# Kernel tuning notes

Hardware: AMD Instinct MI355X
Metric: run time of the kernel (lower is better)

Reference implementation:

```python
import jax, jax.numpy as jnp
import numpy as np

NINPUT = 16
NHIDDEN = 256
NHAGE = 256
NOUT = 8
NSTEP = 501
BATCH = 256
FP_ITERS = 100  # Picard iterations replacing scipy.fsolve equilibrium solve


def setup_inputs() -> dict:
    key = jax.random.key(0)
    ks = jax.random.split(key, 14)
    def rn(k, shape, s):
        return jax.random.normal(k, shape, dtype=jnp.float32) * s
    D = NINPUT * NHIDDEN + NHIDDEN * NHIDDEN + NHIDDEN
    return {
        "u": rn(ks[0], (BATCH, NSTEP, NINPUT + 1), 1.0),
        # aging GRU (PyTorch nn.GRU, 1 layer, batch_first)
        "gru_Wih": rn(ks[1], (3 * NHAGE, NINPUT + 1), 0.05),
        "gru_Whh": rn(ks[2], (3 * NHAGE, NHAGE), 0.05),
        "gru_bih": rn(ks[3], (3 * NHAGE,), 0.05),
        "gru_bhh": rn(ks[4], (3 * NHAGE,), 0.05),
        # linearage: nhidden_age -> D (small scale so dparams are perturbations)
        "Wage": rn(ks[5], (D, NHAGE), 0.01),
        "bage": rn(ks[6], (D,), 0.01),
        # base RNN cell params (tanh cell: tanh(A x + B u + C))
        "Wih": rn(ks[7], (NHIDDEN, NINPUT), 0.05),
        "Whh": rn(ks[8], (NHIDDEN, NHIDDEN), 0.05),
        "bih": rn(ks[9], (NHIDDEN,), 0.05),
        "bhh": rn(ks[10], (NHIDDEN,), 0.05),
        "tau": rn(ks[11], (NHIDDEN,), 0.1),
        # output head
        "Wout": rn(ks[12], (NOUT, NHIDDEN), 0.05),
        "bout": rn(ks[13], (NOUT,), 0.05),
    }


def reference(u, gru_Wih, gru_Whh, gru_bih, gru_bhh, Wage, bage,
              Wih, Whh, bih, bhh, tau, Wout, bout):
    B, T, _ = u.shape
    nI, nH = NINPUT, NHIDDEN

    # ---- aging GRU over full input (feature dim == ninput+1), h0 = 0 ----
    def gru_step(h, xt):
        gi = xt @ gru_Wih.T + gru_bih        # [B, 3*Hage]
        gh = h @ gru_Whh.T + gru_bhh
        ir, iz, inn = jnp.split(gi, 3, axis=-1)
        hr, hz, hn = jnp.split(gh, 3, axis=-1)
        r = jax.nn.sigmoid(ir + hr)
        z = jax.nn.sigmoid(iz + hz)
        n = jnp.tanh(inn + r * hn)
        return (1.0 - z) * n + z * h, None

    h0 = jnp.zeros((B, NHAGE), u.dtype)
    hT, _ = jax.lax.scan(gru_step, h0, jnp.swapaxes(u, 0, 1))
    dparams = hT @ Wage.T + bage             # [B, D]

    # ---- per-sample parameter perturbations (param_update, rnn branch) ----
    Dwu = dparams[:, : nI * nH].reshape(B, nH, nI)
    Dwr = dparams[:, nI * nH : nI * nH + nH * nH].reshape(B, nH, nH)
    Dbu = dparams[:, nI * nH + nH * nH :]
    A = Whh + Dwr                            # [B, H, H]
    Bm = Wih + Dwu                           # [B, H, I]
    C = bih + bhh + Dbu                      # [B, H]

    un = u[:, :, :nI]                        # ODE drive signal
    et = jnp.exp(tau)
    Bu = jnp.einsum('bhi,bti->bth', Bm, un)  # precompute B@u(t): [B, T, H]

    # ---- equilibrium init (rnnzero): x = exp(tau) * tanh(A x + B u0 + C) ----
    def fp(i, x):
        return et * jnp.tanh(jnp.einsum('bhk,bk->bh', A, x) + Bu[:, 0] + C)
    x0 = jax.lax.fori_loop(0, FP_ITERS, fp, jnp.zeros((B, nH), u.dtype))

    # ---- fixed-step Euler on integer grid t=0..T-1 (dt=1); u(t_k)=u[:,k] ----
    def euler(x, bu_k):
        xn = x + jnp.tanh(jnp.einsum('bhk,bk->bh', A, x) + bu_k + C) - x / et
        return xn, xn
    _, xs = jax.lax.scan(euler, x0, jnp.swapaxes(Bu[:, :-1], 0, 1))
    traj = jnp.swapaxes(jnp.concatenate([x0[None], xs], axis=0), 0, 1)  # [B,T,H]

    return traj @ Wout.T + bout              # [B, T, noutput]
```

## Files before the change

### kernel.cpp

```cpp
#include <hip/hip_runtime.h>
#include <hip/hip_bf16.h>

#define BATCH  256
#define TSTEPS 501
#define NIN1   17
#define NH     256
#define DPAR   69888
#define KAUG   288
#define HKAUG  144
#define FPIT   100

typedef _Float16 f16;
typedef f16   f16x2  __attribute__((ext_vector_type(2)));
typedef f16   f16x8  __attribute__((ext_vector_type(8)));
typedef short bf16x8 __attribute__((ext_vector_type(8)));
typedef float f32x4  __attribute__((ext_vector_type(4)));

__device__ __forceinline__ float dot2(unsigned w, unsigned v, float c) {
#if __has_builtin(__builtin_amdgcn_fdot2)
  return __builtin_amdgcn_fdot2(__builtin_bit_cast(f16x2, w), __builtin_bit_cast(f16x2, v), c, false);
#else
  f16x2 a = __builtin_bit_cast(f16x2, w), b = __builtin_bit_cast(f16x2, v);
  return c + (float)a[0] * (float)b[0] + (float)a[1] * (float)b[1];
#endif
}

__device__ __forceinline__ unsigned packh2(float a, float b) {
  f16x2 v; v[0] = (f16)a; v[1] = (f16)b;
  return __builtin_bit_cast(unsigned, v);
}

__device__ __forceinline__ short f2bf(float x) {
  __hip_bfloat16 b = __float2bfloat16(x);
  return __builtin_bit_cast(short, b);
}
__device__ __forceinline__ float bfs2f(short s) {
  return __bfloat162float(__builtin_bit_cast(__hip_bfloat16, s));
}

__device__ __forceinline__ float sigm(float x) { return 1.f / (1.f + __expf(-x)); }
__device__ __forceinline__ float tanh_f(float x) {
  float e = __expf(2.f * x);
  return 1.f - 2.f / (e + 1.f);
}

__global__ __launch_bounds__(512, 1) void gru_kernel(
    const float* __restrict__ u,
    const float* __restrict__ gWih,
    const float* __restrict__ gWhh,
    const float* __restrict__ gbih,
    const float* __restrict__ gbhh,
    short* __restrict__ A2)
{
  const int b   = blockIdx.x;
  const int tid = threadIdx.x;
  const int j   = tid & 255;
  const int hf  = tid >> 8;

  __shared__ __align__(16) unsigned vecu[KAUG / 2];
  __shared__ float part_r[NH], part_z[NH], part_nh[NH], part_ni[NH];
  __shared__ __align__(16) f16 ubuf[TSTEPS * NIN1 + 15];

  {
    const float* ub = u + (size_t)b * TSTEPS * NIN1;
    for (int idx = tid; idx < TSTEPS * NIN1; idx += 512)
      ubuf[idx] = (f16)ub[idx];
  }

  unsigned wr[72], wz[72], wnh[72], wni[9];

  auto augw = [&](int g, int k) -> float {
    if (k < NH) return gWhh[g * NH + k];
    if (k < NH + NIN1) return gWih[g * NIN1 + (k - NH)];
    return 0.f;
  };

#pragma unroll
  for (int p = 0; p < 72; ++p) {
    int k = hf * HKAUG + 2 * p;
    wr[p] = packh2(augw(j, k), augw(j, k + 1));
    wz[p] = packh2(augw(j + 256, k), augw(j + 256, k + 1));
    float n0 = (k     < NH) ? gWhh[(j + 512) * NH + k]     : 0.f;
    float n1 = (k + 1 < NH) ? gWhh[(j + 512) * NH + k + 1] : 0.f;
    wnh[p] = packh2(n0, n1);
  }
#pragma unroll
  for (int p = 0; p < 9; ++p) {
    float a = 0.f, c = 0.f;
    if (hf == 1) {
      a = gWih[(j + 512) * NIN1 + 2 * p];
      if (2 * p + 1 < NIN1) c = gWih[(j + 512) * NIN1 + 2 * p + 1];
    }
    wni[p] = packh2(a, c);
  }
  const float bias_r  = gbih[j]       + gbhh[j];
  const float bias_z  = gbih[j + 256] + gbhh[j + 256];
  const float bias_in = gbih[j + 512];
  const float bias_hn = gbhh[j + 512];

  float h = 0.f;
  {
    f16* vech = (f16*)vecu;
    if (hf == 0) vech[j] = (f16)0.f;
    else if (j < 32) vech[NH + j] = (f16)0.f;
  }
  __syncthreads();
  if (hf == 0 && j < NIN1) ((f16*)vecu)[NH + j] = ubuf[j];
  __syncthreads();

  for (int t = 0; t < TSTEPS; ++t) {
    f16 xnext = (f16)0.f;
    if (hf == 0 && j < NIN1 && t + 1 < TSTEPS)
      xnext = ubuf[(t + 1) * NIN1 + j];

    float accR = 0.f, accZ = 0.f, accNH = 0.f, accNI = 0.f;
    const uint4* v4 = (const uint4*)(vecu + hf * (HKAUG / 2));
#pragma unroll
    for (int c = 0; c < 18; ++c) {
      uint4 v = v4[c];
      accR  = dot2(wr[4 * c + 0], v.x, accR);
      accR  = dot2(wr[4 * c + 1], v.y, accR);
      accR  = dot2(wr[4 * c + 2], v.z, accR);
      accR  = dot2(wr[4 * c + 3], v.w, accR);
      accZ  = dot2(wz[4 * c + 0], v.x, accZ);
      accZ  = dot2(wz[4 * c + 1], v.y, accZ);
      accZ  = dot2(wz[4 * c + 2], v.z, accZ);
      accZ  = dot2(wz[4 * c + 3], v.w, accZ);
      accNH = dot2(wnh[4 * c + 0], v.x, accNH);
      accNH = dot2(wnh[4 * c + 1], v.y, accNH);
      accNH = dot2(wnh[4 * c + 2], v.z, accNH);
      accNH = dot2(wnh[4 * c + 3], v.w, accNH);
    }
    if (hf == 1) {
      const uint4* vi = (const uint4*)(vecu + 128);
      uint4 va = vi[0], vb = vi[1];
      accNI = dot2(wni[0], va.x, accNI);
      accNI = dot2(wni[1], va.y, accNI);
      accNI = dot2(wni[2], va.z, accNI);
      accNI = dot2(wni[3], va.w, accNI);
      accNI = dot2(wni[4], vb.x, accNI);
      accNI = dot2(wni[5], vb.y, accNI);
      accNI = dot2(wni[6], vb.z, accNI);
      accNI = dot2(wni[7], vb.w, accNI);
      accNI = dot2(wni[8], vecu[136], accNI);
      part_r[j] = accR; part_z[j] = accZ; part_nh[j] = accNH; part_ni[j] = accNI;
    }
    __syncthreads();
    if (hf == 0) {
      float rp  = accR  + part_r[j]  + bias_r;
      float zp  = accZ  + part_z[j]  + bias_z;
      float hn  = accNH + part_nh[j] + bias_hn;
      float inn = part_ni[j] + bias_in;
      float r = sigm(rp), z = sigm(zp);
      float n = tanh_f(inn + r * hn);
      h = (1.f - z) * n + z * h;
      f16* vech = (f16*)vecu;
      vech[j] = (f16)h;
      if (j < NIN1) vech[NH + j] = xnext;
    }
    __syncthreads();
  }

  if (hf == 0) {
    short hi = f2bf(h);
    A2[(size_t)b * 512 + j]       = hi;
    A2[(size_t)b * 512 + 256 + j] = f2bf(h - bfs2f(hi));
  }
}

__global__ __launch_bounds__(256, 2) void gemm_kernel(
    const short* __restrict__ A2,
    const float* __restrict__ Wage,
    const float* __restrict__ bage,
    const float* __restrict__ Wih,
    const float* __restrict__ Whh,
    const float* __restrict__ bih,
    const float* __restrict__ bhh,
    f16* __restrict__ dp, int mb, int nb)
{
  __shared__ __align__(16) short As[128 * 40];
  __shared__ __align__(16) short Bs[128 * 40];
  const int tid = threadIdx.x;
  const int n0 = blockIdx.x * 128, m0 = blockIdx.y * 128;
  const int w = tid >> 6, l = tid & 63;
  const int wm = w & 1, wn = w >> 1;
  const int lm = l & 15, lq = l >> 4;

  f32x4 acc[4][4] = {};

  for (int k0 = 0; k0 < 512; k0 += 32) {
    const int ksrc = k0 & 255;
#pragma unroll
    for (int r = 0; r < 2; ++r) {
      int idx = r * 256 + tid;
      int row = idx >> 2, q = idx & 3;
      int rowg = mb + m0 + row; if (rowg > 255) rowg = 255;
      *((uint4*)(As + row * 40 + q * 8)) =
          *((const uint4*)(A2 + (size_t)rowg * 512 + k0 + q * 8));
      const float* wsrc = Wage + (size_t)(n0 + row) * 256 + ksrc + q * 8;
      f32x4 w0 = *((const f32x4*)wsrc);
      f32x4 w1 = *((const f32x4*)(wsrc + 4));
      bf16x8 pk;
      pk[0] = f2bf(w0[0]); pk[1] = f2bf(w0[1]); pk[2] = f2bf(w0[2]); pk[3] = f2bf(w0[3]);
      pk[4] = f2bf(w1[0]); pk[5] = f2bf(w1[1]); pk[6] = f2bf(w1[2]); pk[7] = f2bf(w1[3]);
      *((bf16x8*)(Bs + row * 40 + q * 8)) = pk;
    }
    __syncthreads();
    bf16x8 af[4], bfr[4];
#pragma unroll
    for (int i = 0; i < 4; ++i)
      af[i] = *((const bf16x8*)(As + (wm * 64 + i * 16 + lm) * 40 + lq * 8));
#pragma unroll
    for (int i = 0; i < 4; ++i)
      bfr[i] = *((const bf16x8*)(Bs + (wn * 64 + i * 16 + lm) * 40 + lq * 8));
#pragma unroll
    for (int i = 0; i < 4; ++i)
#pragma unroll
      for (int jn = 0; jn < 4; ++jn)
        acc[i][jn] = __builtin_amdgcn_mfma_f32_16x16x32_bf16(af[i], bfr[jn], acc[i][jn], 0, 0, 0);
    __syncthreads();
  }

  float addv[4];
#pragma unroll
  for (int jn = 0; jn < 4; ++jn) {
    int d = n0 + wn * 64 + jn * 16 + lm;
    float a = bage[d];
    if (d < 4096)       a += Wih[d];
    else if (d < 69632) a += Whh[d - 4096];
    else                a += bih[d - 69632] + bhh[d - 69632];
    addv[jn] = a;
  }

#pragma unroll
  for (int i = 0; i < 4; ++i)
#pragma unroll
    for (int jn = 0; jn < 4; ++jn)
#pragma unroll
      for (int rr = 0; rr < 4; ++rr) {
        int mloc = m0 + wm * 64 + i * 16 + lq * 4 + rr;
        int n = n0 + wn * 64 + jn * 16 + lm;
        if (mloc < nb)
          dp[(size_t)mloc * DPAR + n] = (f16)(acc[i][jn][rr] + addv[jn]);
      }
}

__global__ __launch_bounds__(256, 1) void dyn_kernel(
    const f16* __restrict__ dp, int mb,
    const float* __restrict__ u,
    const float* __restrict__ tau,
    const float* __restrict__ Wout,
    const float* __restrict__ bout,
    float* __restrict__ out)
{
  const int b = mb + blockIdx.x;
  const int j = threadIdx.x;
  const f16* __restrict__ base = dp + (size_t)blockIdx.x * DPAR;

  __shared__ __align__(16) unsigned xbuf[2][128];
  __shared__ __align__(16) unsigned uf[TSTEPS * 8];
  __shared__ __align__(16) float ob[TSTEPS * 8];

  {
    f16* uf16 = (f16*)uf;
    const float* ub = u + (size_t)b * TSTEPS * NIN1;
    for (int idx = j; idx < TSTEPS * 16; idx += 256) {
      int t = idx >> 4, i = idx & 15;
      uf16[idx] = (f16)ub[t * NIN1 + i];
    }
  }

  uint4 Ah[32];
#pragma unroll
  for (int c = 0; c < 32; ++c)
    Ah[c] = *((const uint4*)(base + 4096 + j * 256 + c * 8));
  uint4 Bh0 = *((const uint4*)(base + j * 16));
  uint4 Bh1 = *((const uint4*)(base + j * 16 + 8));
  const float Cc = (float)base[69632 + j];
  const float et = __expf(tau[j]);
  const float inv_et = 1.f / et;

  const int l = j & 63, wv = j >> 6;
  const int po = 2 * wv + (l >> 5), ps = l & 31;
  uint4 wseg;
  {
    const float* wp = Wout + po * 256 + ps * 8;
    wseg.x = packh2(wp[0], wp[1]); wseg.y = packh2(wp[2], wp[3]);
    wseg.z = packh2(wp[4], wp[5]); wseg.w = packh2(wp[6], wp[7]);
  }
  const float bo = bout[po];

  if (j < 128) { xbuf[0][j] = 0u; xbuf[1][j] = 0u; }
  __syncthreads();

  auto bu_at = [&](int t) -> float {
    const uint4* up = (const uint4*)(uf + t * 8);
    uint4 ua = up[0], ub4 = up[1];
    float s0 = dot2(Bh0.x, ua.x, 0.f);  s0 = dot2(Bh0.y, ua.y, s0);
    s0 = dot2(Bh0.z, ua.z, s0);         s0 = dot2(Bh0.w, ua.w, s0);
    float s1 = dot2(Bh1.x, ub4.x, 0.f); s1 = dot2(Bh1.y, ub4.y, s1);
    s1 = dot2(Bh1.z, ub4.z, s1);        s1 = dot2(Bh1.w, ub4.w, s1);
    return s0 + s1;
  };
  const float bu0 = bu_at(0);

  int cur = 0;
  float x = 0.f;
  for (int it = 0; it < FPIT; ++it) {
    float a0 = 0.f, a1 = 0.f, a2 = 0.f, a3 = 0.f;
    const uint4* xp = (const uint4*)xbuf[cur];
#pragma unroll
    for (int c = 0; c < 32; ++c) {
      uint4 v = xp[c];
      a0 = dot2(Ah[c].x, v.x, a0);
      a1 = dot2(Ah[c].y, v.y, a1);
      a2 = dot2(Ah[c].z, v.z, a2);
      a3 = dot2(Ah[c].w, v.w, a3);
    }
    x = et * tanh_f(bu0 + Cc + ((a0 + a1) + (a2 + a3)));
    ((f16*)xbuf[cur ^ 1])[j] = (f16)x;
    __syncthreads();
    cur ^= 1;
  }

  auto project = [&](int t) {
    const uint4* xp = (const uint4*)xbuf[cur];
    uint4 v = xp[ps];
    float p = dot2(wseg.x, v.x, 0.f);
    p = dot2(wseg.y, v.y, p);
    p = dot2(wseg.z, v.z, p);
    p = dot2(wseg.w, v.w, p);
    p += __shfl_down(p, 16, 32);
    p += __shfl_down(p, 8, 32);
    p += __shfl_down(p, 4, 32);
    p += __shfl_down(p, 2, 32);
    p += __shfl_down(p, 1, 32);
    if (ps == 0) ob[t * 8 + po] = p + bo;
  };

  for (int k = 0; k < TSTEPS - 1; ++k) {
    float bu = bu_at(k);
    float a0 = 0.f, a1 = 0.f, a2 = 0.f, a3 = 0.f;
    const uint4* xp = (const uint4*)xbuf[cur];
#pragma unroll
    for (int c = 0; c < 32; ++c) {
      uint4 v = xp[c];
      a0 = dot2(Ah[c].x, v.x, a0);
      a1 = dot2(Ah[c].y, v.y, a1);
      a2 = dot2(Ah[c].z, v.z, a2);
      a3 = dot2(Ah[c].w, v.w, a3);
    }
    float xn = x + tanh_f(bu + Cc + ((a0 + a1) + (a2 + a3))) - x * inv_et;
    ((f16*)xbuf[cur ^ 1])[j] = (f16)xn;
    project(k);
    x = xn;
    __syncthreads();
    cur ^= 1;
  }
  project(TSTEPS - 1);
  __syncthreads();

  {
    float* og = out + (size_t)b * TSTEPS * 8;
    for (int idx = j; idx < TSTEPS * 8; idx += 256) og[idx] = ob[idx];
  }
}

extern "C" void kernel_launch(void* const* d_in, const int* in_sizes, int n_in,
                              void* d_out, int out_size, void* d_ws, size_t ws_size,
                              hipStream_t stream)
{
  const float* u    = (const float*)d_in[0];
  const float* gWih = (const float*)d_in[1];
  const float* gWhh = (const float*)d_in[2];
  const float* gbih = (const float*)d_in[3];
  const float* gbhh = (const float*)d_in[4];
  const float* Wage = (const float*)d_in[5];
  const float* bage = (const float*)d_in[6];
  const float* Wih  = (const float*)d_in[7];
  const float* Whh  = (const float*)d_in[8];
  const float* bih  = (const float*)d_in[9];
  const float* bhh  = (const float*)d_in[10];
  const float* tau  = (const float*)d_in[11];
  const float* Wout = (const float*)d_in[12];
  const float* bout = (const float*)d_in[13];
  float* out = (float*)d_out;

  const size_t A2_BYTES = (size_t)BATCH * 512 * 2;
  size_t a2_off = (ws_size > A2_BYTES + 4096)
                    ? ((ws_size - A2_BYTES) & ~(size_t)255) : 0;
  short* A2 = (short*)((char*)d_ws + a2_off);
  f16* dp = (f16*)d_ws;

  int bpc = (int)(a2_off / ((size_t)DPAR * sizeof(f16)));
  if (bpc < 1)     bpc = 1;
  if (bpc > BATCH) bpc = BATCH;

  gru_kernel<<<BATCH, 512, 0, stream>>>(u, gWih, gWhh, gbih, gbhh, A2);

  for (int mb = 0; mb < BATCH; mb += bpc) {
    int nb = BATCH - mb; if (nb > bpc) nb = bpc;
    dim3 gg(DPAR / 128, (nb + 127) / 128);
    gemm_kernel<<<gg, 256, 0, stream>>>(A2, Wage, bage, Wih, Whh, bih, bhh, dp, mb, nb);
    dyn_kernel<<<nb, 256, 0, stream>>>(dp, mb, u, tau, Wout, bout, out);
  }
}
```

Baseline: 1.551 ms.

## Split GRU recurrence K dimension across four thread groups per block

The GRU kernel now runs 1024 threads per block instead of 512. Each of four 256-thread groups handles a quarter of the augmented K range and writes partial sums to shared memory, where they are reduced. This halves per-thread register weights and the serial dot-product chain per timestep, aiming to cut per-step latency in the sequential recurrence. The cost is more LDS traffic, a larger reduction, and the input-gate weights moved to LDS; a 1024-thread block with many registers may pressure occupancy.

Measured after the change: 1.877 ms. 1.21x slower.

```diff
diff --git a/kernel.cpp b/kernel.cpp
--- a/kernel.cpp
+++ b/kernel.cpp
@@ -7,7 +7,6 @@
 #define NH     256
 #define DPAR   69888
 #define KAUG   288
-#define HKAUG  144
 #define FPIT   100
 
 typedef _Float16 f16;
@@ -44,7 +43,7 @@
   return 1.f - 2.f / (e + 1.f);
 }
 
-__global__ __launch_bounds__(512, 1) void gru_kernel(
+__global__ __launch_bounds__(1024, 1) void gru_kernel(
     const float* __restrict__ u,
     const float* __restrict__ gWih,
     const float* __restrict__ gWhh,
@@ -55,19 +54,18 @@
   const int b   = blockIdx.x;
   const int tid = threadIdx.x;
   const int j   = tid & 255;
-  const int hf  = tid >> 8;
+  const int q   = tid >> 8;
 
   __shared__ __align__(16) unsigned vecu[KAUG / 2];
-  __shared__ float part_r[NH], part_z[NH], part_nh[NH], part_ni[NH];
+  __shared__ float part_r[4][NH], part_z[4][NH], part_nh[4][NH], part_ni[NH];
   __shared__ __align__(16) f16 ubuf[TSTEPS * NIN1 + 15];
+  __shared__ unsigned wniLDS[NH * 9];
 
   {
     const float* ub = u + (size_t)b * TSTEPS * NIN1;
-    for (int idx = tid; idx < TSTEPS * NIN1; idx += 512)
+    for (int idx = tid; idx < TSTEPS * NIN1; idx += 1024)
       ubuf[idx] = (f16)ub[idx];
   }
-
-  unsigned wr[72], wz[72], wnh[72], wni[9];
 
   auto augw = [&](int g, int k) -> float {
     if (k < NH) return gWhh[g * NH + k];
@@ -75,48 +73,49 @@
     return 0.f;
   };
 
-#pragma unroll
-  for (int p = 0; p < 72; ++p) {
-    int k = hf * HKAUG + 2 * p;
+  unsigned wr[36], wz[36], wnh[36];
+  const int k0q = 72 * q;
+#pragma unroll
+  for (int p = 0; p < 36; ++p) {
+    int k = k0q + 2 * p;
     wr[p] = packh2(augw(j, k), augw(j, k + 1));
     wz[p] = packh2(augw(j + 256, k), augw(j + 256, k + 1));
     float n0 = (k     < NH) ? gWhh[(j + 512) * NH + k]     : 0.f;
     float n1 = (k + 1 < NH) ? gWhh[(j + 512) * NH + k + 1] : 0.f;
     wnh[p] = packh2(n0, n1);
   }
-#pragma unroll
-  for (int p = 0; p < 9; ++p) {
-    float a = 0.f, c = 0.f;
-    if (hf == 1) {
-      a = gWih[(j + 512) * NIN1 + 2 * p];
-      if (2 * p + 1 < NIN1) c = gWih[(j + 512) * NIN1 + 2 * p + 1];
-    }
-    wni[p] = packh2(a, c);
-  }
-  const float bias_r  = gbih[j]       + gbhh[j];
-  const float bias_z  = gbih[j + 256] + gbhh[j + 256];
-  const float bias_in = gbih[j + 512];
-  const float bias_hn = gbhh[j + 512];
+
+  float bias_own;
+  if      (q == 0) bias_own = gbih[j]       + gbhh[j];
+  else if (q == 1) bias_own = gbih[j + 256] + gbhh[j + 256];
+  else if (q == 2) bias_own = gbhh[j + 512];
+  else             bias_own = gbih[j + 512];
+
+  if (q == 3) {
+#pragma unroll
+    for (int p = 0; p < 9; ++p) {
+      float a = gWih[(j + 512) * NIN1 + 2 * p];
+      float c = (2 * p + 1 < NIN1) ? gWih[(j + 512) * NIN1 + 2 * p + 1] : 0.f;
+      wniLDS[j * 9 + p] = packh2(a, c);
+    }
+  }
+
+  if (q == 0) ((f16*)vecu)[j] = (f16)0.f;
+  if (q == 1 && j < 32) ((f16*)vecu)[NH + j] = (f16)0.f;
+  __syncthreads();
+  if (q == 0 && j < NIN1) ((f16*)vecu)[NH + j] = ubuf[j];
+  __syncthreads();
 
   float h = 0.f;
-  {
-    f16* vech = (f16*)vecu;
-    if (hf == 0) vech[j] = (f16)0.f;
-    else if (j < 32) vech[NH + j] = (f16)0.f;
-  }
-  __syncthreads();
-  if (hf == 0 && j < NIN1) ((f16*)vecu)[NH + j] = ubuf[j];
-  __syncthreads();
-
   for (int t = 0; t < TSTEPS; ++t) {
     f16 xnext = (f16)0.f;
-    if (hf == 0 && j < NIN1 && t + 1 < TSTEPS)
+    if (q == 0 && j < NIN1 && t + 1 < TSTEPS)
       xnext = ubuf[(t + 1) * NIN1 + j];
 
-    float accR = 0.f, accZ = 0.f, accNH = 0.f, accNI = 0.f;
-    const uint4* v4 = (const uint4*)(vecu + hf * (HKAUG / 2));
-#pragma unroll
-    for (int c = 0; c < 18; ++c) {
+    float accR = 0.f, accZ = 0.f, accNH = 0.f;
+    const uint4* v4 = (const uint4*)(vecu + 36 * q);
+#pragma unroll
+    for (int c = 0; c < 9; ++c) {
       uint4 v = v4[c];
       accR  = dot2(wr[4 * c + 0], v.x, accR);
       accR  = dot2(wr[4 * c + 1], v.y, accR);
@@ -131,26 +130,28 @@
       accNH = dot2(wnh[4 * c + 2], v.z, accNH);
       accNH = dot2(wnh[4 * c + 3], v.w, accNH);
     }
-    if (hf == 1) {
-      const uint4* vi = (const uint4*)(vecu + 128);
-      uint4 va = vi[0], vb = vi[1];
-      accNI = dot2(wni[0], va.x, accNI);
-      accNI = dot2(wni[1], va.y, accNI);
-      accNI = dot2(wni[2], va.z, accNI);
-      accNI = dot2(wni[3], va.w, accNI);
-      accNI = dot2(wni[4], vb.x, accNI);
-      accNI = dot2(wni[5], vb.y, accNI);
-      accNI = dot2(wni[6], vb.z, accNI);
-      accNI = dot2(wni[7], vb.w, accNI);
-      accNI = dot2(wni[8], vecu[136], accNI);
-      part_r[j] = accR; part_z[j] = accZ; part_nh[j] = accNH; part_ni[j] = accNI;
-    }
-    __syncthreads();
-    if (hf == 0) {
-      float rp  = accR  + part_r[j]  + bias_r;
-      float zp  = accZ  + part_z[j]  + bias_z;
-      float hn  = accNH + part_nh[j] + bias_hn;
-      float inn = part_ni[j] + bias_in;
+    if (q == 3) {
+      float accNI = 0.f;
+#pragma unroll
+      for (int p = 0; p < 9; ++p)
+        accNI = dot2(wniLDS[j * 9 + p], vecu[128 + p], accNI);
+      part_ni[j]    = accNI + bias_own;
+      part_r[3][j]  = accR;
+      part_z[3][j]  = accZ;
+      part_nh[3][j] = accNH;
+    } else if (q == 2) {
+      part_r[2][j] = accR; part_z[2][j] = accZ; part_nh[2][j] = accNH + bias_own;
+    } else if (q == 1) {
+      part_r[1][j] = accR; part_z[1][j] = accZ + bias_own; part_nh[1][j] = accNH;
+    } else {
+      part_r[0][j] = accR + bias_own; part_z[0][j] = accZ; part_nh[0][j] = accNH;
+    }
+    __syncthreads();
+    if (q == 0) {
+      float rp  = (part_r[0][j]  + part_r[1][j])  + (part_r[2][j]  + part_r[3][j]);
+      float zp  = (part_z[0][j]  + part_z[1][j])  + (part_z[2][j]  + part_z[3][j]);
+      float hn  = (part_nh[0][j] + part_nh[1][j]) + (part_nh[2][j] + part_nh[3][j]);
+      float inn = part_ni[j];
       float r = sigm(rp), z = sigm(zp);
       float n = tanh_f(inn + r * hn);
       h = (1.f - z) * n + z * h;
@@ -161,7 +162,7 @@
     __syncthreads();
   }
 
-  if (hf == 0) {
+  if (q == 0) {
     short hi = f2bf(h);
     A2[(size_t)b * 512 + j]       = hi;
     A2[(size_t)b * 512 + 256 + j] = f2bf(h - bfs2f(hi));
@@ -193,17 +194,17 @@
 #pragma unroll
     for (int r = 0; r < 2; ++r) {
       int idx = r * 256 + tid;
-      int row = idx >> 2, q = idx & 3;
+      int row = idx >> 2, qq = idx & 3;
       int rowg = mb + m0 + row; if (rowg > 255) rowg = 255;
-      *((uint4*)(As + row * 40 + q * 8)) =
-          *((const uint4*)(A2 + (size_t)rowg * 512 + k0 + q * 8));
-      const float* wsrc = Wage + (size_t)(n0 + row) * 256 + ksrc + q * 8;
+      *((uint4*)(As + row * 40 + qq * 8)) =
+          *((const uint4*)(A2 + (size_t)rowg * 512 + k0 + qq * 8));
+      const float* wsrc = Wage + (size_t)(n0 + row) * 256 + ksrc + qq * 8;
       f32x4 w0 = *((const f32x4*)wsrc);
       f32x4 w1 = *((const f32x4*)(wsrc + 4));
       bf16x8 pk;
       pk[0] = f2bf(w0[0]); pk[1] = f2bf(w0[1]); pk[2] = f2bf(w0[2]); pk[3] = f2bf(w0[3]);
       pk[4] = f2bf(w1[0]); pk[5] = f2bf(w1[1]); pk[6] = f2bf(w1[2]); pk[7] = f2bf(w1[3]);
-      *((bf16x8*)(Bs + row * 40 + q * 8)) = pk;
+      *((bf16x8*)(Bs + row * 40 + qq * 8)) = pk;
     }
     __syncthreads();
     bf16x8 af[4], bfr[4];
@@ -396,7 +397,7 @@
   if (bpc < 1)     bpc = 1;
   if (bpc > BATCH) bpc = BATCH;
 
-  gru_kernel<<<BATCH, 512, 0, stream>>>(u, gWih, gWhh, gbih, gbhh, A2);
+  gru_kernel<<<BATCH, 1024, 0, stream>>>(u, gWih, gWhh, gbih, gbhh, A2);
 
   for (int mb = 0; mb < BATCH; mb += bpc) {
     int nb = BATCH - mb; if (nb > bpc) nb = bpc;
```
